# Kernel tuning notes

Hardware: AMD Instinct MI355X
Metric: run time of the kernel (lower is better)

## Reference

```python
import jax, jax.numpy as jnp
import numpy as np

B, F, H, D, TE, CE = 16384, 1024, 64, 256, 4, 4

def setup_inputs() -> dict:
    key = jax.random.key(0)
    ks = iter(jax.random.split(key, 40))
    s = 0.02
    mk = lambda shape: jax.random.normal(next(ks), shape, jnp.float32) * s
    inp = {
        'x_A': jax.random.normal(next(ks), (B, F), jnp.float32),
        'x_S': jax.random.normal(next(ks), (B, F), jnp.float32),
        'x_B': jax.random.normal(next(ks), (B, F), jnp.float32),
        # stacked per-expert weights for the three expert groups (A, Shared, B)
        'W1A': mk((TE, F, H)), 'b1A': mk((TE, H)), 'W2A': mk((TE, H, D)), 'b2A': mk((TE, D)),
        'W1S': mk((CE, F, H)), 'b1S': mk((CE, H)), 'W2S': mk((CE, H, D)), 'b2S': mk((CE, D)),
        'W1B': mk((TE, F, H)), 'b1B': mk((TE, H)), 'W2B': mk((TE, H, D)), 'b2B': mk((TE, D)),
        # gate weights
        'WgA': mk((F, TE + CE)), 'bgA': mk((TE + CE,)),
        'WgB': mk((F, TE + CE)), 'bgB': mk((TE + CE,)),
        'WgS': mk((F, 2 * TE + CE)), 'bgS': mk((2 * TE + CE,)),
    }
    return inp

def _expert_group(x, W1, b1, W2, b2):
    # x: [B,F], W1: [E,F,H] -> [B,E,H]; W2: [E,H,D] -> [B,E,D]
    h = jax.nn.relu(jnp.einsum('bf,efh->beh', x, W1) + b1)  # dropout p=0 -> identity
    return jax.nn.relu(jnp.einsum('beh,ehd->bed', h, W2) + b2)

def reference(x_A, x_S, x_B,
              W1A, b1A, W2A, b2A,
              W1S, b1S, W2S, b2S,
              W1B, b1B, W2B, b2B,
              WgA, bgA, WgB, bgB, WgS, bgS):
    EA = _expert_group(x_A, W1A, b1A, W2A, b2A)  # [B,TE,D]
    ES = _expert_group(x_S, W1S, b1S, W2S, b2S)  # [B,CE,D]
    EB = _expert_group(x_B, W1B, b1B, W2B, b2B)  # [B,TE,D]
    gA = jax.nn.softmax(x_A @ WgA + bgA, axis=1)  # [B,TE+CE]
    gS = jax.nn.softmax(x_S @ WgS + bgS, axis=1)  # [B,2TE+CE]
    gB = jax.nn.softmax(x_B @ WgB + bgB, axis=1)  # [B,TE+CE]
    outA = jnp.einsum('bed,be->bd', jnp.concatenate([EA, ES], axis=1), gA)
    outS = jnp.einsum('bed,be->bd', jnp.concatenate([EA, ES, EB], axis=1), gS)
    outB = jnp.einsum('bed,be->bd', jnp.concatenate([EB, ES], axis=1), gB)
    return (outA, outS, outB)
```

## Files before the change

kernel.cpp:

```cpp
#include <hip/hip_runtime.h>


#define BB 16384
#define FF 1024

typedef _Float16 f16;
typedef __fp16 h16x2 __attribute__((ext_vector_type(2)));
typedef _Float16 f16x4 __attribute__((ext_vector_type(4)));
typedef _Float16 f16x8 __attribute__((ext_vector_type(8)));
typedef float f32x4 __attribute__((ext_vector_type(4)));

__device__ __forceinline__ void load_lds16(const void* g, void* l) {
    __builtin_amdgcn_global_load_lds(
        (const __attribute__((address_space(1))) unsigned int*)g,
        (__attribute__((address_space(3))) unsigned int*)l, 16, 0, 0);
}

__device__ __forceinline__ f16x8 pack8(float4 lo, float4 hi) {
    union { f16x8 v; h16x2 p[4]; } u;
    u.p[0] = __builtin_amdgcn_cvt_pkrtz(lo.x, lo.y);
    u.p[1] = __builtin_amdgcn_cvt_pkrtz(lo.z, lo.w);
    u.p[2] = __builtin_amdgcn_cvt_pkrtz(hi.x, hi.y);
    u.p[3] = __builtin_amdgcn_cvt_pkrtz(hi.z, hi.w);
    return u.v;
}

#define SBAR() __builtin_amdgcn_sched_barrier(0)

__global__ __launch_bounds__(256) void pack_kernel(
    const float* __restrict__ W1A, const float* __restrict__ W1S, const float* __restrict__ W1B,
    const float* __restrict__ W2A, const float* __restrict__ W2S, const float* __restrict__ W2B,
    const float* __restrict__ WgA, const float* __restrict__ WgS, const float* __restrict__ WgB,
    f16* __restrict__ Wp, f16* __restrict__ W2T, f16* __restrict__ Gp)
{
    __shared__ float T[64 * 65];
    const int b = blockIdx.x, tid = threadIdx.x;

    if (b < 192) {
        int g = b >> 6, e = (b >> 4) & 3, k0 = (b & 15) * 64;
        const float* W1 = (g == 0) ? W1A : ((g == 1) ? W1S : W1B);
        const float* src = W1 + e * 65536 + k0 * 64;
#pragma unroll
        for (int r = 0; r < 4; ++r) {
            int slot = r * 256 + tid, kr = slot >> 4, h4 = slot & 15;
            float4 v = *(const float4*)(src + kr * 64 + h4 * 4);
            T[(h4 * 4 + 0) * 65 + kr] = v.x;
            T[(h4 * 4 + 1) * 65 + kr] = v.y;
            T[(h4 * 4 + 2) * 65 + kr] = v.z;
            T[(h4 * 4 + 3) * 65 + kr] = v.w;
        }
        __syncthreads();
        f16* dst = Wp + g * 262144 + e * 64 * 1024 + k0;
#pragma unroll
        for (int r = 0; r < 4; ++r) {
            int slot = r * 256 + tid, h = slot >> 4, k4 = slot & 15;
            f16x4 o;
            o[0] = (f16)T[h * 65 + k4 * 4 + 0];
            o[1] = (f16)T[h * 65 + k4 * 4 + 1];
            o[2] = (f16)T[h * 65 + k4 * 4 + 2];
            o[3] = (f16)T[h * 65 + k4 * 4 + 3];
            *(f16x4*)(dst + h * 1024 + k4 * 4) = o;
        }
    } else if (b < 240) {
        int bb = b - 192;
        int g = bb >> 4, e = (bb >> 2) & 3, d0 = (bb & 3) * 64;
        const float* W2 = (g == 0) ? W2A : ((g == 1) ? W2S : W2B);
        const float* src = W2 + e * 16384 + d0;
#pragma unroll
        for (int r = 0; r < 4; ++r) {
            int slot = r * 256 + tid, hr = slot >> 4, d4 = slot & 15;
            float4 v = *(const float4*)(src + hr * 256 + d4 * 4);
            T[(d4 * 4 + 0) * 65 + hr] = v.x;
            T[(d4 * 4 + 1) * 65 + hr] = v.y;
            T[(d4 * 4 + 2) * 65 + hr] = v.z;
            T[(d4 * 4 + 3) * 65 + hr] = v.w;
        }
        __syncthreads();
        f16* dst = W2T + (g * 4 + e) * 16384 + d0 * 64;
#pragma unroll
        for (int r = 0; r < 4; ++r) {
            int slot = r * 256 + tid, dl = slot >> 4, h4 = slot & 15;
            f16x4 o;
            o[0] = (f16)T[dl * 65 + h4 * 4 + 0];
            o[1] = (f16)T[dl * 65 + h4 * 4 + 1];
            o[2] = (f16)T[dl * 65 + h4 * 4 + 2];
            o[3] = (f16)T[dl * 65 + h4 * 4 + 3];
            *(f16x4*)(dst + dl * 64 + h4 * 4) = o;
        }
    } else {
        int g = b - 240;
        int ng = (g == 1) ? 12 : 8;
        const float* Wg = (g == 0) ? WgA : ((g == 1) ? WgS : WgB);
#pragma unroll 4
        for (int r = 0; r < 64; ++r) {
            int j = r * 256 + tid;
            int kt = j >> 9, c = (j >> 5) & 15, kk = j & 31;
            Gp[g * 16384 + j] = (c < ng) ? (f16)Wg[(kt * 32 + kk) * ng + c] : (f16)0.0f;
        }
    }
}

__global__ __launch_bounds__(256) void l1_kernel(
    const float* __restrict__ xA, const float* __restrict__ xS, const float* __restrict__ xB,
    const float* __restrict__ b1A, const float* __restrict__ b1S, const float* __restrict__ b1B,
    const float* __restrict__ bgA, const float* __restrict__ bgS, const float* __restrict__ bgB,
    const f16* __restrict__ Wp,
    const f16* __restrict__ Gp,
    f16* __restrict__ hbuf,
    float* __restrict__ gates)
{
    const int g = blockIdx.z;
    const float* x  = (g == 0) ? xA  : ((g == 1) ? xS  : xB);
    const float* b1 = (g == 0) ? b1A : ((g == 1) ? b1S : b1B);
    const float* bg = (g == 0) ? bgA : ((g == 1) ? bgS : bgB);
    const int ng = (g == 1) ? 12 : 8;
    float* gout = gates + ((g == 0) ? (size_t)0
                         : (g == 1) ? (size_t)BB * 8
                                    : (size_t)BB * 8 + (size_t)BB * 12);

    const int row0 = blockIdx.y * 128;
    const int col0 = blockIdx.x * 128;
    const bool do_gate = (blockIdx.x == 0);

    __shared__ __align__(16) float Asf[2][128 * 32];
    __shared__ __align__(16) f16   Bsh[2][128 * 32];
    __shared__ __align__(16) f16   Gs[2][512];

    const int tid  = threadIdx.x;
    const int lane = tid & 63;
    const int wave = tid >> 6;
    const int wm = (wave >> 1) * 64;
    const int wn = (wave & 1) * 64;
    const int lrow = lane & 15;
    const int quad = lane >> 4;

    const f16* Wgrp = Wp + (size_t)g * 256 * 1024;
    const f16* Ggrp = Gp + (size_t)g * 16384;

    f32x4 acc[4][4] = {};
    f32x4 gacc[4] = {};
    const bool my_gate = do_gate && ((wave & 1) == 0);

    auto stage_g = [&](int t, int buf) {
        if (do_gate)
            load_lds16(Ggrp + (size_t)t * 512 + lane * 8, &Gs[buf][lane * 8]);
    };
    auto stage_ab = [&](int t, int buf) {
        int k0 = t * 32;
#pragma unroll
        for (int r = 0; r < 4; ++r) {
            int s = r * 256 + tid;
            int m = s >> 3, slot = s & 7;
            int seg = slot ^ (m & 7);
            load_lds16(x + (size_t)(row0 + m) * FF + k0 + seg * 4, &Asf[buf][s * 4]);
        }
#pragma unroll
        for (int r = 0; r < 2; ++r) {
            int s = r * 256 + tid;
            int m = s >> 2, slot = s & 3;
            int seg = slot ^ ((m >> 1) & 3);
            load_lds16(Wgrp + (size_t)(col0 + m) * FF + k0 + seg * 8, &Bsh[buf][s * 8]);
        }
    };

    stage_g(0, 0);
    SBAR();
    stage_ab(0, 0);
    SBAR();

    for (int t = 0; t < 32; ++t) {
        const int cur = t & 1;
        if (t < 31) {
            stage_g(t + 1, cur ^ 1);
            SBAR();
            stage_ab(t + 1, cur ^ 1);
            SBAR();
            if (do_gate) { asm volatile("s_waitcnt vmcnt(7) lgkmcnt(0)" ::: "memory"); }
            else         { asm volatile("s_waitcnt vmcnt(6) lgkmcnt(0)" ::: "memory"); }
        } else {
            asm volatile("s_waitcnt vmcnt(0) lgkmcnt(0)" ::: "memory");
        }
        SBAR();
        __builtin_amdgcn_s_barrier();
        SBAR();

        f16x8 af[4], bfr[4];
#pragma unroll
        for (int i = 0; i < 4; ++i) {
            int m = wm + i * 16 + lrow;
            const float* rp = &Asf[cur][m * 32];
            int s0 = (2 * quad) ^ (m & 7);
            int s1 = s0 ^ 1;
            float4 lo = *(const float4*)(rp + s0 * 4);
            float4 hi = *(const float4*)(rp + s1 * 4);
            af[i] = pack8(lo, hi);
        }
#pragma unroll
        for (int j = 0; j < 4; ++j) {
            int n = wn + j * 16 + lrow;
            int slot = quad ^ ((n >> 1) & 3);
            bfr[j] = *(const f16x8*)(&Bsh[cur][n * 32 + slot * 8]);
        }
#pragma unroll
        for (int i = 0; i < 4; ++i)
#pragma unroll
            for (int j = 0; j < 4; ++j)
                acc[i][j] = __builtin_amdgcn_mfma_f32_16x16x32_f16(af[i], bfr[j], acc[i][j], 0, 0, 0);
        if (my_gate) {
            f16x8 gb = *(const f16x8*)(&Gs[cur][lrow * 32 + quad * 8]);
#pragma unroll
            for (int i = 0; i < 4; ++i)
                gacc[i] = __builtin_amdgcn_mfma_f32_16x16x32_f16(af[i], gb, gacc[i], 0, 0, 0);
        }
        asm volatile("s_waitcnt lgkmcnt(0)" ::: "memory");
        SBAR();
        __builtin_amdgcn_s_barrier();
        SBAR();
    }

#pragma unroll
    for (int j = 0; j < 4; ++j) {
        int c = col0 + wn + j * 16 + lrow;
        float bias = b1[c];
#pragma unroll
        for (int i = 0; i < 4; ++i) {
#pragma unroll
            for (int r = 0; r < 4; ++r) {
                int row = row0 + wm + i * 16 + quad * 4 + r;
                float v = fmaxf(acc[i][j][r] + bias, 0.0f);
                hbuf[((size_t)g * BB + row) * 256 + c] = (f16)v;
            }
        }
    }

    if (my_gate) {
        int c = lrow;
        bool valid = (c < ng);
        float bias = valid ? bg[c] : 0.0f;
#pragma unroll
        for (int i = 0; i < 4; ++i) {
#pragma unroll
            for (int r = 0; r < 4; ++r) {
                int row = row0 + wm + i * 16 + quad * 4 + r;
                float logit = valid ? (gacc[i][r] + bias) : -1e30f;
                float mx = logit;
#pragma unroll
                for (int m = 1; m < 16; m <<= 1)
                    mx = fmaxf(mx, __shfl_xor(mx, m, 16));
                float ev = valid ? __expf(logit - mx) : 0.0f;
                float sum = ev;
#pragma unroll
                for (int m = 1; m < 16; m <<= 1)
                    sum += __shfl_xor(sum, m, 16);
                if (valid) gout[(size_t)row * ng + c] = ev / sum;
            }
        }
    }
}

__global__ __launch_bounds__(256) void l2_kernel(
    const f16* __restrict__ hbuf,
    const f16* __restrict__ W2T,
    const float* __restrict__ b2A, const float* __restrict__ b2S, const float* __restrict__ b2B,
    const float* __restrict__ gates,
    float* __restrict__ out)
{
    const int o = blockIdx.y;
    const int row0 = blockIdx.x * 64;
    const int tid = threadIdx.x;
    const int lane = tid & 63;
    const int wave = tid >> 6;
    const int wn = wave * 64;
    const int lrow = lane & 15;
    const int quad = lane >> 4;

    const int ng = (o == 1) ? 12 : 8;
    const float* gp = gates + ((o == 0) ? (size_t)0
                             : (o == 1) ? (size_t)BB * 8
                                        : (size_t)BB * 8 + (size_t)BB * 12);

    __shared__ __align__(16) f16 Ash[2][64 * 64];
    __shared__ __align__(16) f16 Bsh[256 * 64];
    __shared__ float gsh[64 * 12];

    auto group_of = [&](int k) -> int {
        if (o == 0)      return (k < 4) ? 0 : 1;
        else if (o == 1) return k >> 2;
        else             return (k < 4) ? 2 : 1;
    };

    auto stage_h = [&](int k, int buf) {
        int gi = group_of(k), e = k & 3;
        const f16* hs = hbuf + ((size_t)gi * BB + row0) * 256 + e * 64;
#pragma unroll
        for (int r = 0; r < 2; ++r) {
            int s = r * 256 + tid;
            int m = s >> 3, slot = s & 7;
            int seg = slot ^ (m & 7);
            load_lds16(hs + (size_t)m * 256 + seg * 8, &Ash[buf][s * 8]);
        }
    };
    auto stage_w2 = [&](int k) {
        int gi = group_of(k), e = k & 3;
        const f16* w2 = W2T + (size_t)(gi * 4 + e) * 256 * 64;
#pragma unroll
        for (int r = 0; r < 8; ++r) {
            int s = r * 256 + tid;
            int m = s >> 3, slot = s & 7;
            int seg = slot ^ (m & 7);
            load_lds16(w2 + (size_t)m * 64 + seg * 8, &Bsh[s * 8]);
        }
    };

    for (int idx = tid; idx < 64 * ng; idx += 256)
        gsh[idx] = gp[(size_t)(row0 + idx / ng) * ng + (idx % ng)];
    SBAR();
    stage_h(0, 0);
    SBAR();

    f32x4 oacc[4][4] = {};

    for (int k = 0; k < ng; ++k) {
        const int cur = k & 1;
        const int gi = group_of(k), e = k & 3;
        const float* b2 = (gi == 0) ? b2A : ((gi == 1) ? b2S : b2B);

        float bias4[4];
#pragma unroll
        for (int j = 0; j < 4; ++j)
            bias4[j] = b2[e * 256 + wn + j * 16 + lrow];
        SBAR();

        stage_w2(k);
        SBAR();
        if (k + 1 < ng) {
            stage_h(k + 1, cur ^ 1);
            SBAR();
            asm volatile("s_waitcnt vmcnt(2) lgkmcnt(0)" ::: "memory");
        } else {
            asm volatile("s_waitcnt vmcnt(0) lgkmcnt(0)" ::: "memory");
        }
        SBAR();
        __builtin_amdgcn_s_barrier();
        SBAR();

        f32x4 eacc[4][4] = {};
#pragma unroll
        for (int kk = 0; kk < 2; ++kk) {
            f16x8 af[4], bfr[4];
#pragma unroll
            for (int i = 0; i < 4; ++i) {
                int rr = i * 16 + lrow;
                int slot = (kk * 4 + quad) ^ (rr & 7);
                af[i] = *(const f16x8*)(&Ash[cur][rr * 64 + slot * 8]);
            }
#pragma unroll
            for (int j = 0; j < 4; ++j) {
                int n = wn + j * 16 + lrow;
                int slot = (kk * 4 + quad) ^ (n & 7);
                bfr[j] = *(const f16x8*)(&Bsh[n * 64 + slot * 8]);
            }
#pragma unroll
            for (int i = 0; i < 4; ++i)
#pragma unroll
                for (int j = 0; j < 4; ++j)
                    eacc[i][j] = __builtin_amdgcn_mfma_f32_16x16x32_f16(af[i], bfr[j], eacc[i][j], 0, 0, 0);
        }

#pragma unroll
        for (int j = 0; j < 4; ++j) {
            float bias = bias4[j];
#pragma unroll
            for (int i = 0; i < 4; ++i) {
#pragma unroll
                for (int r = 0; r < 4; ++r) {
                    int rl = i * 16 + quad * 4 + r;
                    float v = fmaxf(eacc[i][j][r] + bias, 0.0f);
                    oacc[i][j][r] += gsh[rl * ng + k] * v;
                }
            }
        }
        asm volatile("s_waitcnt lgkmcnt(0)" ::: "memory");
        SBAR();
        __builtin_amdgcn_s_barrier();
        SBAR();
    }

#pragma unroll
    for (int j = 0; j < 4; ++j) {
        int d = wn + j * 16 + lrow;
#pragma unroll
        for (int i = 0; i < 4; ++i) {
#pragma unroll
            for (int r = 0; r < 4; ++r) {
                int rl = i * 16 + quad * 4 + r;
                out[((size_t)o * BB + row0 + rl) * 256 + d] = oacc[i][j][r];
            }
        }
    }
}

extern "C" void kernel_launch(void* const* d_in, const int* in_sizes, int n_in,
                              void* d_out, int out_size, void* d_ws, size_t ws_size,
                              hipStream_t stream)
{
    (void)in_sizes; (void)n_in; (void)out_size; (void)ws_size;

    const float* xA  = (const float*)d_in[0];
    const float* xS  = (const float*)d_in[1];
    const float* xB  = (const float*)d_in[2];
    const float* W1A = (const float*)d_in[3];
    const float* b1A = (const float*)d_in[4];
    const float* W2A = (const float*)d_in[5];
    const float* b2A = (const float*)d_in[6];
    const float* W1S = (const float*)d_in[7];
    const float* b1S = (const float*)d_in[8];
    const float* W2S = (const float*)d_in[9];
    const float* b2S = (const float*)d_in[10];
    const float* W1B = (const float*)d_in[11];
    const float* b1B = (const float*)d_in[12];
    const float* W2B = (const float*)d_in[13];
    const float* b2B = (const float*)d_in[14];
    const float* WgA = (const float*)d_in[15];
    const float* bgA = (const float*)d_in[16];
    const float* WgB = (const float*)d_in[17];
    const float* bgB = (const float*)d_in[18];
    const float* WgS = (const float*)d_in[19];
    const float* bgS = (const float*)d_in[20];

    char* ws = (char*)d_ws;
    f16*   Wp   = (f16*)(ws);
    f16*   W2T  = (f16*)(ws + 0x180000);
    f16*   Gp   = (f16*)(ws + 0x1E0000);
    f16*   hbuf = (f16*)(ws + 0x200000);
    float* gate = (float*)(ws + 0x200000 + 0x1800000);

    pack_kernel<<<243, 256, 0, stream>>>(W1A, W1S, W1B, W2A, W2S, W2B,
                                         WgA, WgS, WgB, Wp, W2T, Gp);
    l1_kernel<<<dim3(2, 128, 3), 256, 0, stream>>>(
        xA, xS, xB, b1A, b1S, b1B, bgA, bgS, bgB,
        Wp, Gp, hbuf, gate);
    l2_kernel<<<dim3(256, 3), 256, 0, stream>>>(
        hbuf, W2T, b2A, b2S, b2B, gate, (float*)d_out);
}
```

Before: 368.2 us.

## Shrink L1 tiles with block swizzle and fuse L2 outputs per row tile

The L1 GEMM drops from 128-row to 64-row tiles with single-buffered LDS and plain __syncthreads, adds a launch-bounds occupancy hint, and remaps block ids so consecutive blocks are spread across groups and row tiles. L2 is restructured so each block loads all three hidden groups for 32 rows into LDS once and accumulates all three outputs (A, S, B) together. This removes the threefold rereading of shared expert activations and weights, and W2 fragments now stream from global into registers with one-step prefetch. In exchange, L1 loses its double-buffered load/compute overlap, and L2 needs about 64 KB of dynamic shared memory and more accumulator registers.

```diff
diff --git a/kernel.cpp b/kernel.cpp
--- a/kernel.cpp
+++ b/kernel.cpp
@@ -24,8 +24,6 @@
     u.p[3] = __builtin_amdgcn_cvt_pkrtz(hi.z, hi.w);
     return u.v;
 }
-
-#define SBAR() __builtin_amdgcn_sched_barrier(0)
 
 __global__ __launch_bounds__(256) void pack_kernel(
     const float* __restrict__ W1A, const float* __restrict__ W1S, const float* __restrict__ W1B,
@@ -100,7 +98,7 @@
     }
 }
 
-__global__ __launch_bounds__(256) void l1_kernel(
+__global__ __launch_bounds__(256, 4) void l1_kernel(
     const float* __restrict__ xA, const float* __restrict__ xS, const float* __restrict__ xB,
     const float* __restrict__ b1A, const float* __restrict__ b1S, const float* __restrict__ b1B,
     const float* __restrict__ bgA, const float* __restrict__ bgS, const float* __restrict__ bgB,
@@ -109,7 +107,14 @@
     f16* __restrict__ hbuf,
     float* __restrict__ gates)
 {
-    const int g = blockIdx.z;
+    int bid = blockIdx.x + (blockIdx.y << 1) + (blockIdx.z << 9);
+    int logical = (bid & 7) * 192 + (bid >> 3);
+    const int lx = logical & 1;
+    const int row0 = ((logical >> 1) & 0xFF) * 64;
+    const int g = logical >> 9;
+    const int col0 = lx * 128;
+    const bool do_gate = (lx == 0);
+
     const float* x  = (g == 0) ? xA  : ((g == 1) ? xS  : xB);
     const float* b1 = (g == 0) ? b1A : ((g == 1) ? b1S : b1B);
     const float* bg = (g == 0) ? bgA : ((g == 1) ? bgS : bgB);
@@ -118,18 +123,14 @@
                          : (g == 1) ? (size_t)BB * 8
                                     : (size_t)BB * 8 + (size_t)BB * 12);
 
-    const int row0 = blockIdx.y * 128;
-    const int col0 = blockIdx.x * 128;
-    const bool do_gate = (blockIdx.x == 0);
-
-    __shared__ __align__(16) float Asf[2][128 * 32];
-    __shared__ __align__(16) f16   Bsh[2][128 * 32];
-    __shared__ __align__(16) f16   Gs[2][512];
+    __shared__ __align__(16) float Asf[64 * 32];
+    __shared__ __align__(16) f16   Bsh[128 * 32];
+    __shared__ __align__(16) f16   Gs[512];
 
     const int tid  = threadIdx.x;
     const int lane = tid & 63;
     const int wave = tid >> 6;
-    const int wm = (wave >> 1) * 64;
+    const int wm = (wave >> 1) * 32;
     const int wn = (wave & 1) * 64;
     const int lrow = lane & 15;
     const int quad = lane >> 4;
@@ -137,85 +138,58 @@
     const f16* Wgrp = Wp + (size_t)g * 256 * 1024;
     const f16* Ggrp = Gp + (size_t)g * 16384;
 
-    f32x4 acc[4][4] = {};
-    f32x4 gacc[4] = {};
+    f32x4 acc[2][4] = {};
+    f32x4 gacc[2] = {};
     const bool my_gate = do_gate && ((wave & 1) == 0);
 
-    auto stage_g = [&](int t, int buf) {
-        if (do_gate)
-            load_lds16(Ggrp + (size_t)t * 512 + lane * 8, &Gs[buf][lane * 8]);
-    };
-    auto stage_ab = [&](int t, int buf) {
-        int k0 = t * 32;
-#pragma unroll
-        for (int r = 0; r < 4; ++r) {
+    for (int t = 0; t < 32; ++t) {
+        const int k0 = t * 32;
+#pragma unroll
+        for (int r = 0; r < 2; ++r) {
             int s = r * 256 + tid;
             int m = s >> 3, slot = s & 7;
             int seg = slot ^ (m & 7);
-            load_lds16(x + (size_t)(row0 + m) * FF + k0 + seg * 4, &Asf[buf][s * 4]);
+            load_lds16(x + (size_t)(row0 + m) * FF + k0 + seg * 4, Asf + s * 4);
         }
 #pragma unroll
         for (int r = 0; r < 2; ++r) {
             int s = r * 256 + tid;
             int m = s >> 2, slot = s & 3;
             int seg = slot ^ ((m >> 1) & 3);
-            load_lds16(Wgrp + (size_t)(col0 + m) * FF + k0 + seg * 8, &Bsh[buf][s * 8]);
-        }
-    };
-
-    stage_g(0, 0);
-    SBAR();
-    stage_ab(0, 0);
-    SBAR();
-
-    for (int t = 0; t < 32; ++t) {
-        const int cur = t & 1;
-        if (t < 31) {
-            stage_g(t + 1, cur ^ 1);
-            SBAR();
-            stage_ab(t + 1, cur ^ 1);
-            SBAR();
-            if (do_gate) { asm volatile("s_waitcnt vmcnt(7) lgkmcnt(0)" ::: "memory"); }
-            else         { asm volatile("s_waitcnt vmcnt(6) lgkmcnt(0)" ::: "memory"); }
-        } else {
-            asm volatile("s_waitcnt vmcnt(0) lgkmcnt(0)" ::: "memory");
-        }
-        SBAR();
-        __builtin_amdgcn_s_barrier();
-        SBAR();
-
-        f16x8 af[4], bfr[4];
-#pragma unroll
-        for (int i = 0; i < 4; ++i) {
+            load_lds16(Wgrp + (size_t)(col0 + m) * FF + k0 + seg * 8, Bsh + s * 8);
+        }
+        if (do_gate && tid < 64)
+            load_lds16(Ggrp + (size_t)t * 512 + tid * 8, Gs + tid * 8);
+        __syncthreads();
+
+        f16x8 af[2], bfr[4];
+#pragma unroll
+        for (int i = 0; i < 2; ++i) {
             int m = wm + i * 16 + lrow;
-            const float* rp = &Asf[cur][m * 32];
+            const float* rp = Asf + m * 32;
             int s0 = (2 * quad) ^ (m & 7);
-            int s1 = s0 ^ 1;
             float4 lo = *(const float4*)(rp + s0 * 4);
-            float4 hi = *(const float4*)(rp + s1 * 4);
+            float4 hi = *(const float4*)(rp + (s0 ^ 1) * 4);
             af[i] = pack8(lo, hi);
         }
 #pragma unroll
         for (int j = 0; j < 4; ++j) {
             int n = wn + j * 16 + lrow;
             int slot = quad ^ ((n >> 1) & 3);
-            bfr[j] = *(const f16x8*)(&Bsh[cur][n * 32 + slot * 8]);
-        }
-#pragma unroll
-        for (int i = 0; i < 4; ++i)
+            bfr[j] = *(const f16x8*)(Bsh + n * 32 + slot * 8);
+        }
+#pragma unroll
+        for (int i = 0; i < 2; ++i)
 #pragma unroll
             for (int j = 0; j < 4; ++j)
                 acc[i][j] = __builtin_amdgcn_mfma_f32_16x16x32_f16(af[i], bfr[j], acc[i][j], 0, 0, 0);
         if (my_gate) {
-            f16x8 gb = *(const f16x8*)(&Gs[cur][lrow * 32 + quad * 8]);
-#pragma unroll
-            for (int i = 0; i < 4; ++i)
+            f16x8 gb = *(const f16x8*)(Gs + lrow * 32 + quad * 8);
+#pragma unroll
+            for (int i = 0; i < 2; ++i)
                 gacc[i] = __builtin_amdgcn_mfma_f32_16x16x32_f16(af[i], gb, gacc[i], 0, 0, 0);
         }
-        asm volatile("s_waitcnt lgkmcnt(0)" ::: "memory");
-        SBAR();
-        __builtin_amdgcn_s_barrier();
-        SBAR();
+        __syncthreads();
     }
 
 #pragma unroll
@@ -223,7 +197,7 @@
         int c = col0 + wn + j * 16 + lrow;
         float bias = b1[c];
 #pragma unroll
-        for (int i = 0; i < 4; ++i) {
+        for (int i = 0; i < 2; ++i) {
 #pragma unroll
             for (int r = 0; r < 4; ++r) {
                 int row = row0 + wm + i * 16 + quad * 4 + r;
@@ -238,7 +212,7 @@
         bool valid = (c < ng);
         float bias = valid ? bg[c] : 0.0f;
 #pragma unroll
-        for (int i = 0; i < 4; ++i) {
+        for (int i = 0; i < 2; ++i) {
 #pragma unroll
             for (int r = 0; r < 4; ++r) {
                 int row = row0 + wm + i * 16 + quad * 4 + r;
@@ -258,143 +232,136 @@
     }
 }
 
-__global__ __launch_bounds__(256) void l2_kernel(
+__global__ __launch_bounds__(256, 2) void l2_kernel(
     const f16* __restrict__ hbuf,
     const f16* __restrict__ W2T,
     const float* __restrict__ b2A, const float* __restrict__ b2S, const float* __restrict__ b2B,
     const float* __restrict__ gates,
     float* __restrict__ out)
 {
-    const int o = blockIdx.y;
-    const int row0 = blockIdx.x * 64;
-    const int tid = threadIdx.x;
+    extern __shared__ char smem[];
+    f16*   hls = (f16*)smem;
+    float* b2s = (float*)(smem + 49152);
+    float* gsh = (float*)(smem + 61440);
+
+    const int row0 = blockIdx.x * 32;
+    const int tid  = threadIdx.x;
     const int lane = tid & 63;
-    const int wave = tid >> 6;
-    const int wn = wave * 64;
+    const int w    = tid >> 6;
     const int lrow = lane & 15;
     const int quad = lane >> 4;
-
-    const int ng = (o == 1) ? 12 : 8;
-    const float* gp = gates + ((o == 0) ? (size_t)0
-                             : (o == 1) ? (size_t)BB * 8
-                                        : (size_t)BB * 8 + (size_t)BB * 12);
-
-    __shared__ __align__(16) f16 Ash[2][64 * 64];
-    __shared__ __align__(16) f16 Bsh[256 * 64];
-    __shared__ float gsh[64 * 12];
-
-    auto group_of = [&](int k) -> int {
-        if (o == 0)      return (k < 4) ? 0 : 1;
-        else if (o == 1) return k >> 2;
-        else             return (k < 4) ? 2 : 1;
+    const int wn2  = w * 64;
+
+    const float* gp0 = gates;
+    const float* gp1 = gates + (size_t)BB * 8;
+    const float* gp2 = gates + (size_t)BB * 8 + (size_t)BB * 12;
+
+#pragma unroll
+    for (int gi = 0; gi < 3; ++gi) {
+#pragma unroll
+        for (int r = 0; r < 4; ++r) {
+            int s = r * 256 + tid;
+            int m = s >> 5, slot = s & 31;
+            int seg = slot ^ (m & 7);
+            load_lds16(hbuf + ((size_t)(gi * BB + row0 + m)) * 256 + seg * 8,
+                       hls + gi * 8192 + s * 8);
+        }
+    }
+    load_lds16(b2A + tid * 4, b2s + tid * 4);
+    load_lds16(b2S + tid * 4, b2s + 1024 + tid * 4);
+    load_lds16(b2B + tid * 4, b2s + 2048 + tid * 4);
+#pragma unroll
+    for (int it = 0; it < 4; ++it) {
+        int idx = it * 256 + tid;
+        if (idx < 896) {
+            int row = idx / 28, c = idx % 28;
+            float v;
+            if (c < 8)       v = gp0[(size_t)(row0 + row) * 8 + c];
+            else if (c < 20) v = gp1[(size_t)(row0 + row) * 12 + (c - 8)];
+            else             v = gp2[(size_t)(row0 + row) * 8 + (c - 20)];
+            gsh[idx] = v;
+        }
+    }
+
+    f16x8 wfA[2][4], wfB[2][4];
+    auto issue_wf2 = [&](int p, f16x8 (&wf)[2][4]) {
+        int gi = p >> 2, e = p & 3;
+        const f16* w2 = W2T + (size_t)(gi * 4 + e) * 16384;
+#pragma unroll
+        for (int kk = 0; kk < 2; ++kk)
+#pragma unroll
+            for (int j = 0; j < 4; ++j)
+                wf[kk][j] = *(const f16x8*)(w2 + (size_t)(wn2 + j * 16 + lrow) * 64 + kk * 32 + quad * 8);
     };
 
-    auto stage_h = [&](int k, int buf) {
-        int gi = group_of(k), e = k & 3;
-        const f16* hs = hbuf + ((size_t)gi * BB + row0) * 256 + e * 64;
-#pragma unroll
-        for (int r = 0; r < 2; ++r) {
-            int s = r * 256 + tid;
-            int m = s >> 3, slot = s & 7;
-            int seg = slot ^ (m & 7);
-            load_lds16(hs + (size_t)m * 256 + seg * 8, &Ash[buf][s * 8]);
-        }
-    };
-    auto stage_w2 = [&](int k) {
-        int gi = group_of(k), e = k & 3;
-        const f16* w2 = W2T + (size_t)(gi * 4 + e) * 256 * 64;
-#pragma unroll
-        for (int r = 0; r < 8; ++r) {
-            int s = r * 256 + tid;
-            int m = s >> 3, slot = s & 7;
-            int seg = slot ^ (m & 7);
-            load_lds16(w2 + (size_t)m * 64 + seg * 8, &Bsh[s * 8]);
-        }
-    };
-
-    for (int idx = tid; idx < 64 * ng; idx += 256)
-        gsh[idx] = gp[(size_t)(row0 + idx / ng) * ng + (idx % ng)];
-    SBAR();
-    stage_h(0, 0);
-    SBAR();
-
-    f32x4 oacc[4][4] = {};
-
-    for (int k = 0; k < ng; ++k) {
-        const int cur = k & 1;
-        const int gi = group_of(k), e = k & 3;
-        const float* b2 = (gi == 0) ? b2A : ((gi == 1) ? b2S : b2B);
-
-        float bias4[4];
+    issue_wf2(0, wfA);
+    __syncthreads();
+
+    f32x4 oA[2][4] = {}, oS[2][4] = {}, oB[2][4] = {};
+
+    auto pair_step = [&](int p, f16x8 (&wfC)[2][4], f16x8 (&wfN)[2][4]) {
+        if (p < 11) issue_wf2(p + 1, wfN);
+        const int gi = p >> 2, e = p & 3;
+
+        f32x4 eacc[2][4] = {};
+#pragma unroll
+        for (int kk = 0; kk < 2; ++kk) {
+            f16x8 af[2];
+#pragma unroll
+            for (int i = 0; i < 2; ++i) {
+                int rr = i * 16 + lrow;
+                int slot = (e * 8 + kk * 4 + quad) ^ (rr & 7);
+                af[i] = *(const f16x8*)(hls + gi * 8192 + rr * 256 + slot * 8);
+            }
+#pragma unroll
+            for (int i = 0; i < 2; ++i)
+#pragma unroll
+                for (int j = 0; j < 4; ++j)
+                    eacc[i][j] = __builtin_amdgcn_mfma_f32_16x16x32_f16(af[i], wfC[kk][j], eacc[i][j], 0, 0, 0);
+        }
+
+        float bias[4];
 #pragma unroll
         for (int j = 0; j < 4; ++j)
-            bias4[j] = b2[e * 256 + wn + j * 16 + lrow];
-        SBAR();
-
-        stage_w2(k);
-        SBAR();
-        if (k + 1 < ng) {
-            stage_h(k + 1, cur ^ 1);
-            SBAR();
-            asm volatile("s_waitcnt vmcnt(2) lgkmcnt(0)" ::: "memory");
-        } else {
-            asm volatile("s_waitcnt vmcnt(0) lgkmcnt(0)" ::: "memory");
-        }
-        SBAR();
-        __builtin_amdgcn_s_barrier();
-        SBAR();
-
-        f32x4 eacc[4][4] = {};
-#pragma unroll
-        for (int kk = 0; kk < 2; ++kk) {
-            f16x8 af[4], bfr[4];
-#pragma unroll
-            for (int i = 0; i < 4; ++i) {
-                int rr = i * 16 + lrow;
-                int slot = (kk * 4 + quad) ^ (rr & 7);
-                af[i] = *(const f16x8*)(&Ash[cur][rr * 64 + slot * 8]);
-            }
-#pragma unroll
-            for (int j = 0; j < 4; ++j) {
-                int n = wn + j * 16 + lrow;
-                int slot = (kk * 4 + quad) ^ (n & 7);
-                bfr[j] = *(const f16x8*)(&Bsh[n * 64 + slot * 8]);
-            }
-#pragma unroll
-            for (int i = 0; i < 4; ++i)
-#pragma unroll
-                for (int j = 0; j < 4; ++j)
-                    eacc[i][j] = __builtin_amdgcn_mfma_f32_16x16x32_f16(af[i], bfr[j], eacc[i][j], 0, 0, 0);
-        }
-
-#pragma unroll
-        for (int j = 0; j < 4; ++j) {
-            float bias = bias4[j];
-#pragma unroll
-            for (int i = 0; i < 4; ++i) {
-#pragma unroll
-                for (int r = 0; r < 4; ++r) {
-                    int rl = i * 16 + quad * 4 + r;
-                    float v = fmaxf(eacc[i][j][r] + bias, 0.0f);
-                    oacc[i][j][r] += gsh[rl * ng + k] * v;
+            bias[j] = b2s[gi * 1024 + e * 256 + wn2 + j * 16 + lrow];
+
+#pragma unroll
+        for (int i = 0; i < 2; ++i) {
+#pragma unroll
+            for (int r = 0; r < 4; ++r) {
+                int row = i * 16 + quad * 4 + r;
+                float ga = 0.f, gs = 0.f, gb = 0.f;
+                if (gi == 0)      { ga = gsh[row * 28 + e];      gs = gsh[row * 28 + 8 + e]; }
+                else if (gi == 1) { ga = gsh[row * 28 + 4 + e];  gs = gsh[row * 28 + 12 + e]; gb = gsh[row * 28 + 24 + e]; }
+                else              { gs = gsh[row * 28 + 16 + e]; gb = gsh[row * 28 + 20 + e]; }
+#pragma unroll
+                for (int j = 0; j < 4; ++j) {
+                    float v = fmaxf(eacc[i][j][r] + bias[j], 0.0f);
+                    if (gi == 0)      { oA[i][j][r] += ga * v; oS[i][j][r] += gs * v; }
+                    else if (gi == 1) { oA[i][j][r] += ga * v; oS[i][j][r] += gs * v; oB[i][j][r] += gb * v; }
+                    else              { oS[i][j][r] += gs * v; oB[i][j][r] += gb * v; }
                 }
             }
         }
-        asm volatile("s_waitcnt lgkmcnt(0)" ::: "memory");
-        SBAR();
-        __builtin_amdgcn_s_barrier();
-        SBAR();
+    };
+
+#pragma unroll
+    for (int pp = 0; pp < 6; ++pp) {
+        pair_step(2 * pp, wfA, wfB);
+        pair_step(2 * pp + 1, wfB, wfA);
     }
 
 #pragma unroll
     for (int j = 0; j < 4; ++j) {
-        int d = wn + j * 16 + lrow;
-#pragma unroll
-        for (int i = 0; i < 4; ++i) {
+        int d = wn2 + j * 16 + lrow;
+#pragma unroll
+        for (int i = 0; i < 2; ++i) {
 #pragma unroll
             for (int r = 0; r < 4; ++r) {
-                int rl = i * 16 + quad * 4 + r;
-                out[((size_t)o * BB + row0 + rl) * 256 + d] = oacc[i][j][r];
+                int row = row0 + i * 16 + quad * 4 + r;
+                out[((size_t)0 * BB + row) * 256 + d] = oA[i][j][r];
+                out[((size_t)1 * BB + row) * 256 + d] = oS[i][j][r];
+                out[((size_t)2 * BB + row) * 256 + d] = oB[i][j][r];
             }
         }
     }
@@ -437,9 +404,9 @@
 
     pack_kernel<<<243, 256, 0, stream>>>(W1A, W1S, W1B, W2A, W2S, W2B,
                                          WgA, WgS, WgB, Wp, W2T, Gp);
-    l1_kernel<<<dim3(2, 128, 3), 256, 0, stream>>>(
+    l1_kernel<<<dim3(2, 256, 3), 256, 0, stream>>>(
         xA, xS, xB, b1A, b1S, b1B, bgA, bgS, bgB,
         Wp, Gp, hbuf, gate);
-    l2_kernel<<<dim3(256, 3), 256, 0, stream>>>(
+    l2_kernel<<<512, 256, 65024, stream>>>(
         hbuf, W2T, b2A, b2S, b2B, gate, (float*)d_out);
 }
```

Result: slower. 483.5 us (+31.3%).
